# Kernel tuning notes

Hardware: AMD Instinct MI355X
Metric: run time of the kernel (lower is better)

## Reference

```python
import jax, jax.numpy as jnp
import numpy as np

# Faithful JAX port of the approxmatch algorithm (Fan et al. / PyTorch-EMDLoss CUDA kernel):
# iterative soft bipartite matching with annealed temperature levels -4^j for j=8..-1, then 0,
# tracking remaining capacities ('saturation') of both point sets.

EPS = 1e-9

def _approx_match(xyz1, xyz2):
    # xyz1: [B,N,D], xyz2: [B,M,D] -> match: [B,N,M]
    B, n, _ = xyz1.shape
    m = xyz2.shape[1]
    factorl = max(n, m) // n  # capacity per point in set 1
    factorr = max(n, m) // m  # capacity per point in set 2
    # pairwise squared distances [B,N,M]
    d2 = jnp.sum((xyz1[:, :, None, :] - xyz2[:, None, :, :]) ** 2, axis=-1)
    # annealing levels: -4^8, -4^7, ..., -4^-1, 0
    levels = jnp.array([-(4.0 ** j) for j in range(8, -2, -1)] + [0.0],
                       dtype=xyz1.dtype)
    satl0 = jnp.full((B, n), float(factorl), dtype=xyz1.dtype)
    satr0 = jnp.full((B, m), float(factorr), dtype=xyz1.dtype)
    match0 = jnp.zeros((B, n, m), dtype=xyz1.dtype)

    def step(carry, level):
        satl, satr, match = carry
        # soft assignment weights scaled by remaining capacity of set 2
        w = jnp.exp(level * d2) * satr[:, None, :]                      # [B,N,M]
        # row-normalize, scaled by remaining capacity of set 1
        w = w / (jnp.sum(w, axis=2, keepdims=True) + EPS) * satl[:, :, None]
        # column capacity clipping
        ss = jnp.sum(w, axis=1) + EPS                                   # [B,M]
        r = jnp.minimum(satr / ss, 1.0)
        w = w * r[:, None, :]
        satr = jnp.maximum(satr - jnp.sum(w, axis=1), 0.0)
        satl = jnp.maximum(satl - jnp.sum(w, axis=2), 0.0)
        return (satl, satr, match + w), None

    (_, _, match), _ = jax.lax.scan(step, (satl0, satr0, match0), levels)
    return match


def setup_inputs() -> dict:
    key = jax.random.key(0)
    k1, k2 = jax.random.split(key)
    xyz1 = jax.random.normal(k1, (8, 2048, 3), dtype=jnp.float32)
    xyz2 = jax.random.normal(k2, (8, 2048, 3), dtype=jnp.float32)
    return {"xyz1": xyz1, "xyz2": xyz2}


def reference(xyz1, xyz2):
    # EMD cost per batch element: sum_{k,l} match[k,l] * ||x1_k - x2_l||
    match = _approx_match(xyz1, xyz2)                                   # [B,N,M]
    d = jnp.sqrt(jnp.sum((xyz1[:, :, None, :] - xyz2[:, None, :, :]) ** 2,
                         axis=-1))                                      # [B,N,M]
    return jnp.sum(match * d, axis=(1, 2))                              # [B]
```

## Files before the change

kernel.cpp:

```cpp
#include <hip/hip_runtime.h>
#include <math.h>

static constexpr int   B_   = 8;
static constexpr int   N_   = 2048;
static constexpr int   TPB  = 256;
static constexpr int   TILE = 32;
static constexpr int   NBLK = (B_ * N_) / TILE;
static constexpr int   BN   = B_ * N_;
static constexpr float EPS_ = 1e-9f;
static constexpr float LOG2E = 1.4426950408889634f;

#define WS_X1    (ws)
#define WS_X2    (ws + 4*BN)
#define WS_SATL  (ws + 8*BN)
#define WS_SATR  (ws + 9*BN)
#define WS_SCAL  (ws + 10*BN)
#define WS_LSCAL (ws + 11*BN)
#define WS_WLS   (reinterpret_cast<float2*>(ws + 12*BN))
#define WS_WR    (ws + 14*BN)
#define WS_COST  (ws + 15*BN)
#define WS_COSTP (ws + 16*BN)

__global__ void __launch_bounds__(TPB)
emd_init(const float* __restrict__ xyz1, const float* __restrict__ xyz2,
         float* __restrict__ ws)
{
    const int idx = blockIdx.x * TPB + threadIdx.x;
    if (idx >= BN) return;
    float x = xyz1[idx*3], y = xyz1[idx*3+1], z = xyz1[idx*3+2];
    reinterpret_cast<float4*>(WS_X1)[idx] =
        make_float4(x, y, z, fmaf(x,x, fmaf(y,y, z*z)));
    x = xyz2[idx*3]; y = xyz2[idx*3+1]; z = xyz2[idx*3+2];
    reinterpret_cast<float4*>(WS_X2)[idx] =
        make_float4(x, y, z, fmaf(x,x, fmaf(y,y, z*z)));
    WS_SATL[idx] = 1.f;
    WS_SATR[idx] = 1.f;
    WS_COST[idx] = 0.f;
    WS_WLS[idx]  = make_float2(0.f, 0.f);
}

template<int MODE>
__global__ void __launch_bounds__(TPB, (MODE == 2) ? 3 : 4)
emd_pass(float* __restrict__ ws, const float lvlA, const float lvlB)
{
    constexpr int SMEM_BYTES = (MODE == 2) ? (32768 + 16384) : 32768;
    __shared__ __align__(16) char smem[SMEM_BYTES];
    float4* pts  = reinterpret_cast<float4*>(smem);
    float2* aux2 = reinterpret_cast<float2*>(smem + 32768);
    float (*red)[33]  = reinterpret_cast<float(*)[33]>(smem);
    float (*red2)[33] = reinterpret_cast<float(*)[33]>(smem + 64*33*4);

    const int b    = blockIdx.x >> 6;
    const int tile = blockIdx.x & 63;
    const int t    = threadIdx.x;
    const int g    = t & 3;
    const int c    = t >> 2;

    const float4* x1v = reinterpret_cast<const float4*>(WS_X1) + b * N_;
    const float4* x2v = reinterpret_cast<const float4*>(WS_X2) + b * N_;
    const float2* wls = WS_WLS + b * N_;
    const float*  lscal = WS_LSCAL + b * N_;
    const float*  wrp   = WS_WR + b * N_;

    for (int p = t; p < N_; p += TPB) {
        if (MODE == 0) {
            float4 v = x2v[p];
            pts[p] = make_float4(v.x, v.y, v.z, fmaf(lvlB, v.w, wls[p].y));
        } else if (MODE == 1) {
            float4 v = x1v[p];
            pts[p] = make_float4(v.x, v.y, v.z, fmaf(lvlB, v.w, lscal[p]));
        } else if (MODE == 2) {
            float4 v = x2v[p];
            pts[p] = v;
            float2 q = wls[p];
            aux2[p] = make_float2(fmaf(lvlA, v.w, q.x), fmaf(lvlB, v.w, q.y));
        } else {
            float4 v = x2v[p];
            pts[p] = make_float4(v.x, v.y, v.z, wrp[p]);
        }
    }

    const float4* ownv = (MODE == 1) ? x2v : x1v;
    const int ob = tile * TILE + g * 8;
    float kx[8], ky[8], kz[8], kq[8];
#pragma unroll
    for (int j = 0; j < 8; ++j) {
        float4 v = ownv[ob + j];
        if (MODE == 0 || MODE == 1) {
            const float m2lv = -2.f * lvlB;
            kx[j] = m2lv * v.x; ky[j] = m2lv * v.y; kz[j] = m2lv * v.z;
            kq[j] = lvlB * v.w;
        } else if (MODE == 2) {
            kx[j] = -2.f * v.x; ky[j] = -2.f * v.y; kz[j] = -2.f * v.z;
            kq[j] = v.w;
        } else {
            kx[j] = v.x; ky[j] = v.y; kz[j] = v.z; kq[j] = 0.f;
        }
    }
    __syncthreads();

    float s1[8], s2[8], s3[8];
#pragma unroll
    for (int j = 0; j < 8; ++j) { s1[j] = 0.f; s2[j] = 0.f; s3[j] = 0.f; }

    int l = c;
    float4 p = pts[l];
    float2 a;
    if (MODE == 2) a = aux2[l];

    if (MODE == 0 || MODE == 1) {
#pragma unroll 4
        for (int i = 0; i < 32; ++i) {
            const int ln = (l + 64) & (N_ - 1);
            const float4 pn = pts[ln];
#pragma unroll
            for (int j = 0; j < 8; ++j) {
                const float arg = fmaf(kx[j], p.x, fmaf(ky[j], p.y,
                                  fmaf(kz[j], p.z, p.w + kq[j])));
                s1[j] += __builtin_amdgcn_exp2f(arg);
            }
            p = pn; l = ln;
        }
    } else if (MODE == 2) {
#pragma unroll 2
        for (int i = 0; i < 32; ++i) {
            const int ln = (l + 64) & (N_ - 1);
            const float4 pn = pts[ln];
            const float2 an = aux2[ln];
#pragma unroll
            for (int j = 0; j < 8; ++j) {
                const float dq = fmaf(kx[j], p.x, fmaf(ky[j], p.y,
                                 fmaf(kz[j], p.z, kq[j])));
                const float d2 = p.w + dq;
                const float sq = __builtin_amdgcn_sqrtf(fmaxf(d2, 0.f));
                const float eA = __builtin_amdgcn_exp2f(fmaf(lvlA, dq, a.x));
                const float eB = __builtin_amdgcn_exp2f(fmaf(lvlB, dq, a.y));
                s1[j] += eA;
                s2[j]  = fmaf(eA, sq, s2[j]);
                s3[j] += eB;
            }
            p = pn; a = an; l = ln;
        }
    } else {
#pragma unroll 4
        for (int i = 0; i < 32; ++i) {
            const int ln = (l + 64) & (N_ - 1);
            const float4 pn = pts[ln];
#pragma unroll
            for (int j = 0; j < 8; ++j) {
                const float dx = p.x - kx[j], dy = p.y - ky[j], dz = p.z - kz[j];
                const float d2 = fmaf(dx, dx, fmaf(dy, dy, dz * dz));
                const float sq = __builtin_amdgcn_sqrtf(fmaxf(d2, 0.f));
                s2[j] = fmaf(p.w, sq, s2[j]);
            }
            p = pn; l = ln;
        }
    }

#define REDUCE(arr, dst)                                                   \
    {   __syncthreads();                                                   \
        _Pragma("unroll")                                                  \
        for (int j = 0; j < 8; ++j) red[c][g * 8 + j] = arr[j];            \
        __syncthreads();                                                   \
        { const int o = t & 31, sg = t >> 5; float a2 = 0.f;               \
          _Pragma("unroll")                                                \
          for (int k = 0; k < 8; ++k) a2 += red[sg * 8 + k][o];            \
          red2[sg][o] = a2; }                                              \
        __syncthreads();                                                   \
        dst = 0.f;                                                         \
        if (t < TILE) { _Pragma("unroll")                                  \
            for (int sgg = 0; sgg < 8; ++sgg) dst += red2[sgg][t]; } }

    const int gidx = b * N_ + tile * TILE + t;

    if (MODE == 0) {
        float rs1; REDUCE(s1, rs1);
        if (t < TILE) {
            const float sc = WS_SATL[gidx] / (rs1 + EPS_);
            WS_SCAL[gidx]  = sc;
            WS_LSCAL[gidx] = __log2f(sc);
        }
    } else if (MODE == 1) {
        float rs1; REDUCE(s1, rs1);
        if (t < TILE) {
            const float sr  = WS_SATR[gidx];
            const float w1s = sr * rs1;
            const float rr  = fminf(sr / (w1s + EPS_), 1.f);
            const float wrv = sr * rr;
            const float srn = fmaxf(sr - rr * w1s, 0.f);
            WS_SATR[gidx] = srn;
            WS_WR[gidx]   = wrv;
            WS_WLS[gidx + b * N_ * 0] = make_float2(__log2f(wrv), __log2f(srn));
        }
    } else if (MODE == 2) {
        float rs1, rs2, rs3;
        REDUCE(s1, rs1); REDUCE(s2, rs2); REDUCE(s3, rs3);
        if (t < TILE) {
            const float scp = WS_SCAL[gidx];
            const float sln = fmaxf(WS_SATL[gidx] - scp * rs1, 0.f);
            WS_COST[gidx]   = fmaf(scp, rs2, WS_COST[gidx]);
            const float scn = sln / (rs3 + EPS_);
            WS_SATL[gidx]  = sln;
            WS_SCAL[gidx]  = scn;
            WS_LSCAL[gidx] = __log2f(scn);
        }
    } else {
        float rs2; REDUCE(s2, rs2);
        float v = 0.f;
        if (t < TILE)
            v = fmaf(WS_SCAL[gidx], rs2, WS_COST[gidx]);
        if (t < 64) {
#pragma unroll
            for (int k = 16; k >= 1; k >>= 1) v += __shfl_xor(v, k, 64);
            if (t == 0) WS_COSTP[blockIdx.x] = v;
        }
    }
#undef REDUCE
}

__global__ void __launch_bounds__(64)
emd_finish(const float* __restrict__ costp, float* __restrict__ out)
{
    const int b = blockIdx.x;
    const int t = threadIdx.x;
    float v = costp[b * 64 + t];
#pragma unroll
    for (int k = 32; k >= 1; k >>= 1) v += __shfl_xor(v, k, 64);
    if (t == 0) out[b] = v;
}

extern "C" void kernel_launch(void* const* d_in, const int* in_sizes, int n_in,
                              void* d_out, int out_size, void* d_ws, size_t ws_size,
                              hipStream_t stream)
{
    const float* xyz1 = (const float*)d_in[0];
    const float* xyz2 = (const float*)d_in[1];
    float* out = (float*)d_out;
    float* ws  = (float*)d_ws;

    emd_init<<<BN / TPB, TPB, 0, stream>>>(xyz1, xyz2, ws);

    static const float levels[11] = {
        -65536.f, -16384.f, -4096.f, -1024.f, -256.f,
        -64.f, -16.f, -4.f, -1.f, -0.25f, 0.f};

    emd_pass<0><<<NBLK, TPB, 0, stream>>>(ws, 0.f, levels[0] * LOG2E);
    emd_pass<1><<<NBLK, TPB, 0, stream>>>(ws, 0.f, levels[0] * LOG2E);
    for (int lev = 1; lev < 11; ++lev) {
        emd_pass<2><<<NBLK, TPB, 0, stream>>>(ws, levels[lev-1] * LOG2E,
                                                  levels[lev]   * LOG2E);
        emd_pass<1><<<NBLK, TPB, 0, stream>>>(ws, 0.f, levels[lev] * LOG2E);
    }
    emd_pass<3><<<NBLK, TPB, 0, stream>>>(ws, 0.f, 0.f);

    emd_finish<<<B_, 64, 0, stream>>>(WS_COSTP, out);
}
```

Measured before the change: 339.2 us.

## Halve row tile to 16, use packed float2 math, fuse final reduction via atomics

Halves the rows handled per block (16 instead of 32) so each block is split across more threads, doubling the grid to 1024 blocks, and caps occupancy at 4 for every mode. The inner distance math is rewritten with 2-wide vector types so the compiler can emit packed FMA instructions. The MODE 2 LDS footprint is reduced by folding one log term into the point w component. The finish kernel is replaced with atomicAdd into a zero-filled output. The intent is to use the GPU more fully and cut ALU issue per element; the cost is reloading the column points for twice as many blocks, plus nondeterministic float summation order from the atomics.

```diff
diff --git a/kernel.cpp b/kernel.cpp
--- a/kernel.cpp
+++ b/kernel.cpp
@@ -1,11 +1,14 @@
 #include <hip/hip_runtime.h>
 #include <math.h>
+
+typedef float f2 __attribute__((ext_vector_type(2)));
 
 static constexpr int   B_   = 8;
 static constexpr int   N_   = 2048;
 static constexpr int   TPB  = 256;
-static constexpr int   TILE = 32;
-static constexpr int   NBLK = (B_ * N_) / TILE;
+static constexpr int   TILE = 16;
+static constexpr int   BPB  = 128;
+static constexpr int   NBLK = B_ * BPB;
 static constexpr int   BN   = B_ * N_;
 static constexpr float EPS_ = 1e-9f;
 static constexpr float LOG2E = 1.4426950408889634f;
@@ -16,10 +19,10 @@
 #define WS_SATR  (ws + 9*BN)
 #define WS_SCAL  (ws + 10*BN)
 #define WS_LSCAL (ws + 11*BN)
-#define WS_WLS   (reinterpret_cast<float2*>(ws + 12*BN))
+#define WS_LSATR (ws + 12*BN)
+#define WS_LWR   (ws + 13*BN)
 #define WS_WR    (ws + 14*BN)
 #define WS_COST  (ws + 15*BN)
-#define WS_COSTP (ws + 16*BN)
 
 __global__ void __launch_bounds__(TPB)
 emd_init(const float* __restrict__ xyz1, const float* __restrict__ xyz2,
@@ -33,47 +36,81 @@
     x = xyz2[idx*3]; y = xyz2[idx*3+1]; z = xyz2[idx*3+2];
     reinterpret_cast<float4*>(WS_X2)[idx] =
         make_float4(x, y, z, fmaf(x,x, fmaf(y,y, z*z)));
-    WS_SATL[idx] = 1.f;
-    WS_SATR[idx] = 1.f;
-    WS_COST[idx] = 0.f;
-    WS_WLS[idx]  = make_float2(0.f, 0.f);
+    WS_SATL[idx]  = 1.f;
+    WS_SATR[idx]  = 1.f;
+    WS_LSATR[idx] = 0.f;
+    WS_COST[idx]  = 0.f;
+}
+
+template<int NA>
+__device__ __forceinline__ void reduce_multi(float* sc, const float (*s)[8],
+                                             int t, float* rs)
+{
+    const int c = t >> 1, g = t & 1;
+    __syncthreads();
+#pragma unroll
+    for (int a = 0; a < NA; ++a) {
+        float* red = sc + a * 2176;
+#pragma unroll
+        for (int j = 0; j < 8; ++j) red[c*17 + g*8 + j] = s[a][j];
+    }
+    __syncthreads();
+    {
+        const int col = t & 15, seg = t >> 4;
+#pragma unroll
+        for (int a = 0; a < NA; ++a) {
+            const float* red = sc + a * 2176;
+            float v = 0.f;
+#pragma unroll
+            for (int k = 0; k < 8; ++k) v += red[(seg*8 + k)*17 + col];
+            sc[6528 + a*272 + seg*17 + col] = v;
+        }
+    }
+    __syncthreads();
+    if (t < 16) {
+#pragma unroll
+        for (int a = 0; a < NA; ++a) {
+            float r = 0.f;
+#pragma unroll
+            for (int q = 0; q < 16; ++q) r += sc[6528 + a*272 + q*17 + t];
+            rs[a] = r;
+        }
+    }
 }
 
 template<int MODE>
-__global__ void __launch_bounds__(TPB, (MODE == 2) ? 3 : 4)
-emd_pass(float* __restrict__ ws, const float lvlA, const float lvlB)
-{
-    constexpr int SMEM_BYTES = (MODE == 2) ? (32768 + 16384) : 32768;
-    __shared__ __align__(16) char smem[SMEM_BYTES];
+__global__ void __launch_bounds__(TPB, 4)
+emd_pass(float* __restrict__ ws, float* __restrict__ out,
+         const float lvA, const float lvB)
+{
+    constexpr int SMEM = (MODE == 2) ? 40960 : 32768;
+    __shared__ __align__(16) char smem[SMEM];
     float4* pts  = reinterpret_cast<float4*>(smem);
-    float2* aux2 = reinterpret_cast<float2*>(smem + 32768);
-    float (*red)[33]  = reinterpret_cast<float(*)[33]>(smem);
-    float (*red2)[33] = reinterpret_cast<float(*)[33]>(smem + 64*33*4);
-
-    const int b    = blockIdx.x >> 6;
-    const int tile = blockIdx.x & 63;
+    float*  auxB = reinterpret_cast<float*>(smem + 32768);
+    float*  sc   = reinterpret_cast<float*>(smem);
+
+    const int b    = blockIdx.x >> 7;
+    const int tile = blockIdx.x & 127;
     const int t    = threadIdx.x;
-    const int g    = t & 3;
-    const int c    = t >> 2;
 
     const float4* x1v = reinterpret_cast<const float4*>(WS_X1) + b * N_;
     const float4* x2v = reinterpret_cast<const float4*>(WS_X2) + b * N_;
-    const float2* wls = WS_WLS + b * N_;
-    const float*  lscal = WS_LSCAL + b * N_;
-    const float*  wrp   = WS_WR + b * N_;
+    const float* lscal = WS_LSCAL + b * N_;
+    const float* lsatr = WS_LSATR + b * N_;
+    const float* lwr   = WS_LWR   + b * N_;
+    const float* wrp   = WS_WR    + b * N_;
 
     for (int p = t; p < N_; p += TPB) {
         if (MODE == 0) {
             float4 v = x2v[p];
-            pts[p] = make_float4(v.x, v.y, v.z, fmaf(lvlB, v.w, wls[p].y));
+            pts[p] = make_float4(v.x, v.y, v.z, lvB * v.w);
         } else if (MODE == 1) {
             float4 v = x1v[p];
-            pts[p] = make_float4(v.x, v.y, v.z, fmaf(lvlB, v.w, lscal[p]));
+            pts[p] = make_float4(v.x, v.y, v.z, fmaf(lvB, v.w, lscal[p]));
         } else if (MODE == 2) {
             float4 v = x2v[p];
-            pts[p] = v;
-            float2 q = wls[p];
-            aux2[p] = make_float2(fmaf(lvlA, v.w, q.x), fmaf(lvlB, v.w, q.y));
+            pts[p]  = make_float4(v.x, v.y, v.z, fmaf(lvA, v.w, lwr[p]));
+            auxB[p] = fmaf(lvB, v.w, lsatr[p]);
         } else {
             float4 v = x2v[p];
             pts[p] = make_float4(v.x, v.y, v.z, wrp[p]);
@@ -81,20 +118,22 @@
     }
 
     const float4* ownv = (MODE == 1) ? x2v : x1v;
-    const int ob = tile * TILE + g * 8;
-    float kx[8], ky[8], kz[8], kq[8];
-#pragma unroll
-    for (int j = 0; j < 8; ++j) {
-        float4 v = ownv[ob + j];
+    const int ob = tile * TILE + (t & 1) * 8;
+    f2 kx[4], ky[4], kz[4], kc[4];
+#pragma unroll
+    for (int jp = 0; jp < 4; ++jp) {
+        float4 v0 = ownv[ob + 2*jp], v1 = ownv[ob + 2*jp + 1];
         if (MODE == 0 || MODE == 1) {
-            const float m2lv = -2.f * lvlB;
-            kx[j] = m2lv * v.x; ky[j] = m2lv * v.y; kz[j] = m2lv * v.z;
-            kq[j] = lvlB * v.w;
-        } else if (MODE == 2) {
-            kx[j] = -2.f * v.x; ky[j] = -2.f * v.y; kz[j] = -2.f * v.z;
-            kq[j] = v.w;
+            const float m2 = -2.f * lvB;
+            kx[jp] = (f2){m2*v0.x, m2*v1.x};
+            ky[jp] = (f2){m2*v0.y, m2*v1.y};
+            kz[jp] = (f2){m2*v0.z, m2*v1.z};
+            kc[jp] = (f2){lvB*v0.w, lvB*v1.w};
         } else {
-            kx[j] = v.x; ky[j] = v.y; kz[j] = v.z; kq[j] = 0.f;
+            kx[jp] = (f2){-2.f*v0.x, -2.f*v1.x};
+            ky[jp] = (f2){-2.f*v0.y, -2.f*v1.y};
+            kz[jp] = (f2){-2.f*v0.z, -2.f*v1.z};
+            kc[jp] = (f2){v0.w, v1.w};
         }
     }
     __syncthreads();
@@ -103,130 +142,110 @@
 #pragma unroll
     for (int j = 0; j < 8; ++j) { s1[j] = 0.f; s2[j] = 0.f; s3[j] = 0.f; }
 
-    int l = c;
+    int l = t >> 1;
     float4 p = pts[l];
-    float2 a;
-    if (MODE == 2) a = aux2[l];
-
-    if (MODE == 0 || MODE == 1) {
-#pragma unroll 4
-        for (int i = 0; i < 32; ++i) {
-            const int ln = (l + 64) & (N_ - 1);
-            const float4 pn = pts[ln];
-#pragma unroll
-            for (int j = 0; j < 8; ++j) {
-                const float arg = fmaf(kx[j], p.x, fmaf(ky[j], p.y,
-                                  fmaf(kz[j], p.z, p.w + kq[j])));
-                s1[j] += __builtin_amdgcn_exp2f(arg);
+    float  ab = (MODE == 2) ? auxB[l] : 0.f;
+
+#pragma unroll 2
+    for (int i = 0; i < 16; ++i) {
+        const int ln = (l + 128) & (N_ - 1);
+        const float4 pn = pts[ln];
+        float abn = 0.f;
+        if (MODE == 2) abn = auxB[ln];
+
+        const f2 px = (f2){p.x, p.x}, py = (f2){p.y, p.y}, pz = (f2){p.z, p.z};
+        float p2s = 0.f;
+        if (MODE == 2 || MODE == 3)
+            p2s = fmaf(p.x, p.x, fmaf(p.y, p.y, p.z * p.z));
+
+#pragma unroll
+        for (int jp = 0; jp < 4; ++jp) {
+            if (MODE == 0 || MODE == 1) {
+                f2 a = kc[jp] + (f2){p.w, p.w};
+                a = kz[jp] * pz + a;
+                a = ky[jp] * py + a;
+                a = kx[jp] * px + a;
+                s1[2*jp]   += __builtin_amdgcn_exp2f(a.x);
+                s1[2*jp+1] += __builtin_amdgcn_exp2f(a.y);
+            } else if (MODE == 2) {
+                f2 dq = kz[jp] * pz + kc[jp];
+                dq = ky[jp] * py + dq;
+                dq = kx[jp] * px + dq;
+                const float d20 = dq.x + p2s, d21 = dq.y + p2s;
+                const float sq0 = __builtin_amdgcn_sqrtf(fmaxf(d20, 0.f));
+                const float sq1 = __builtin_amdgcn_sqrtf(fmaxf(d21, 0.f));
+                const float eA0 = __builtin_amdgcn_exp2f(fmaf(lvA, dq.x, p.w));
+                const float eA1 = __builtin_amdgcn_exp2f(fmaf(lvA, dq.y, p.w));
+                const float eB0 = __builtin_amdgcn_exp2f(fmaf(lvB, dq.x, ab));
+                const float eB1 = __builtin_amdgcn_exp2f(fmaf(lvB, dq.y, ab));
+                s1[2*jp]   += eA0;            s1[2*jp+1] += eA1;
+                s2[2*jp]    = fmaf(eA0, sq0, s2[2*jp]);
+                s2[2*jp+1]  = fmaf(eA1, sq1, s2[2*jp+1]);
+                s3[2*jp]   += eB0;            s3[2*jp+1] += eB1;
+            } else {
+                f2 dq = kz[jp] * pz + kc[jp];
+                dq = ky[jp] * py + dq;
+                dq = kx[jp] * px + dq;
+                const float sq0 = __builtin_amdgcn_sqrtf(fmaxf(dq.x + p2s, 0.f));
+                const float sq1 = __builtin_amdgcn_sqrtf(fmaxf(dq.y + p2s, 0.f));
+                s2[2*jp]   = fmaf(p.w, sq0, s2[2*jp]);
+                s2[2*jp+1] = fmaf(p.w, sq1, s2[2*jp+1]);
             }
-            p = pn; l = ln;
-        }
-    } else if (MODE == 2) {
-#pragma unroll 2
-        for (int i = 0; i < 32; ++i) {
-            const int ln = (l + 64) & (N_ - 1);
-            const float4 pn = pts[ln];
-            const float2 an = aux2[ln];
-#pragma unroll
-            for (int j = 0; j < 8; ++j) {
-                const float dq = fmaf(kx[j], p.x, fmaf(ky[j], p.y,
-                                 fmaf(kz[j], p.z, kq[j])));
-                const float d2 = p.w + dq;
-                const float sq = __builtin_amdgcn_sqrtf(fmaxf(d2, 0.f));
-                const float eA = __builtin_amdgcn_exp2f(fmaf(lvlA, dq, a.x));
-                const float eB = __builtin_amdgcn_exp2f(fmaf(lvlB, dq, a.y));
-                s1[j] += eA;
-                s2[j]  = fmaf(eA, sq, s2[j]);
-                s3[j] += eB;
-            }
-            p = pn; a = an; l = ln;
-        }
-    } else {
-#pragma unroll 4
-        for (int i = 0; i < 32; ++i) {
-            const int ln = (l + 64) & (N_ - 1);
-            const float4 pn = pts[ln];
-#pragma unroll
-            for (int j = 0; j < 8; ++j) {
-                const float dx = p.x - kx[j], dy = p.y - ky[j], dz = p.z - kz[j];
-                const float d2 = fmaf(dx, dx, fmaf(dy, dy, dz * dz));
-                const float sq = __builtin_amdgcn_sqrtf(fmaxf(d2, 0.f));
-                s2[j] = fmaf(p.w, sq, s2[j]);
-            }
-            p = pn; l = ln;
-        }
-    }
-
-#define REDUCE(arr, dst)                                                   \
-    {   __syncthreads();                                                   \
-        _Pragma("unroll")                                                  \
-        for (int j = 0; j < 8; ++j) red[c][g * 8 + j] = arr[j];            \
-        __syncthreads();                                                   \
-        { const int o = t & 31, sg = t >> 5; float a2 = 0.f;               \
-          _Pragma("unroll")                                                \
-          for (int k = 0; k < 8; ++k) a2 += red[sg * 8 + k][o];            \
-          red2[sg][o] = a2; }                                              \
-        __syncthreads();                                                   \
-        dst = 0.f;                                                         \
-        if (t < TILE) { _Pragma("unroll")                                  \
-            for (int sgg = 0; sgg < 8; ++sgg) dst += red2[sgg][t]; } }
+        }
+        p = pn; ab = abn; l = ln;
+    }
 
     const int gidx = b * N_ + tile * TILE + t;
 
     if (MODE == 0) {
-        float rs1; REDUCE(s1, rs1);
+        float rs[1];
+        reduce_multi<1>(sc, &s1, t, rs);
         if (t < TILE) {
-            const float sc = WS_SATL[gidx] / (rs1 + EPS_);
-            WS_SCAL[gidx]  = sc;
-            WS_LSCAL[gidx] = __log2f(sc);
+            const float scv = WS_SATL[gidx] / (rs[0] + EPS_);
+            WS_SCAL[gidx]  = scv;
+            WS_LSCAL[gidx] = __log2f(scv);
         }
     } else if (MODE == 1) {
-        float rs1; REDUCE(s1, rs1);
+        float rs[1];
+        reduce_multi<1>(sc, &s1, t, rs);
         if (t < TILE) {
             const float sr  = WS_SATR[gidx];
-            const float w1s = sr * rs1;
+            const float w1s = sr * rs[0];
             const float rr  = fminf(sr / (w1s + EPS_), 1.f);
             const float wrv = sr * rr;
             const float srn = fmaxf(sr - rr * w1s, 0.f);
-            WS_SATR[gidx] = srn;
-            WS_WR[gidx]   = wrv;
-            WS_WLS[gidx + b * N_ * 0] = make_float2(__log2f(wrv), __log2f(srn));
+            WS_SATR[gidx]  = srn;
+            WS_WR[gidx]    = wrv;
+            WS_LWR[gidx]   = __log2f(wrv);
+            WS_LSATR[gidx] = __log2f(srn);
         }
     } else if (MODE == 2) {
-        float rs1, rs2, rs3;
-        REDUCE(s1, rs1); REDUCE(s2, rs2); REDUCE(s3, rs3);
+        float sall[3][8];
+#pragma unroll
+        for (int j = 0; j < 8; ++j) {
+            sall[0][j] = s1[j]; sall[1][j] = s2[j]; sall[2][j] = s3[j];
+        }
+        float rs[3];
+        reduce_multi<3>(sc, sall, t, rs);
         if (t < TILE) {
             const float scp = WS_SCAL[gidx];
-            const float sln = fmaxf(WS_SATL[gidx] - scp * rs1, 0.f);
-            WS_COST[gidx]   = fmaf(scp, rs2, WS_COST[gidx]);
-            const float scn = sln / (rs3 + EPS_);
+            const float sln = fmaxf(WS_SATL[gidx] - scp * rs[0], 0.f);
+            WS_COST[gidx]   = fmaf(scp, rs[1], WS_COST[gidx]);
+            const float scn = sln / (rs[2] + EPS_);
             WS_SATL[gidx]  = sln;
             WS_SCAL[gidx]  = scn;
             WS_LSCAL[gidx] = __log2f(scn);
         }
     } else {
-        float rs2; REDUCE(s2, rs2);
-        float v = 0.f;
-        if (t < TILE)
-            v = fmaf(WS_SCAL[gidx], rs2, WS_COST[gidx]);
-        if (t < 64) {
-#pragma unroll
-            for (int k = 16; k >= 1; k >>= 1) v += __shfl_xor(v, k, 64);
-            if (t == 0) WS_COSTP[blockIdx.x] = v;
-        }
-    }
-#undef REDUCE
-}
-
-__global__ void __launch_bounds__(64)
-emd_finish(const float* __restrict__ costp, float* __restrict__ out)
-{
-    const int b = blockIdx.x;
-    const int t = threadIdx.x;
-    float v = costp[b * 64 + t];
-#pragma unroll
-    for (int k = 32; k >= 1; k >>= 1) v += __shfl_xor(v, k, 64);
-    if (t == 0) out[b] = v;
+        float rs[1];
+        reduce_multi<1>(sc, &s2, t, rs);
+        if (t < 16) {
+            float v = fmaf(WS_SCAL[gidx], rs[0], WS_COST[gidx]);
+#pragma unroll
+            for (int k = 8; k >= 1; k >>= 1) v += __shfl_xor(v, k, 16);
+            if (t == 0) atomicAdd(out + b, v);
+        }
+    }
 }
 
 extern "C" void kernel_launch(void* const* d_in, const int* in_sizes, int n_in,
@@ -238,20 +257,19 @@
     float* out = (float*)d_out;
     float* ws  = (float*)d_ws;
 
+    hipMemsetAsync(d_out, 0, B_ * sizeof(float), stream);
     emd_init<<<BN / TPB, TPB, 0, stream>>>(xyz1, xyz2, ws);
 
     static const float levels[11] = {
         -65536.f, -16384.f, -4096.f, -1024.f, -256.f,
         -64.f, -16.f, -4.f, -1.f, -0.25f, 0.f};
 
-    emd_pass<0><<<NBLK, TPB, 0, stream>>>(ws, 0.f, levels[0] * LOG2E);
-    emd_pass<1><<<NBLK, TPB, 0, stream>>>(ws, 0.f, levels[0] * LOG2E);
+    emd_pass<0><<<NBLK, TPB, 0, stream>>>(ws, out, 0.f, levels[0] * LOG2E);
+    emd_pass<1><<<NBLK, TPB, 0, stream>>>(ws, out, 0.f, levels[0] * LOG2E);
     for (int lev = 1; lev < 11; ++lev) {
-        emd_pass<2><<<NBLK, TPB, 0, stream>>>(ws, levels[lev-1] * LOG2E,
-                                                  levels[lev]   * LOG2E);
-        emd_pass<1><<<NBLK, TPB, 0, stream>>>(ws, 0.f, levels[lev] * LOG2E);
-    }
-    emd_pass<3><<<NBLK, TPB, 0, stream>>>(ws, 0.f, 0.f);
-
-    emd_finish<<<B_, 64, 0, stream>>>(WS_COSTP, out);
-}
+        emd_pass<2><<<NBLK, TPB, 0, stream>>>(ws, out, levels[lev-1] * LOG2E,
+                                                       levels[lev]   * LOG2E);
+        emd_pass<1><<<NBLK, TPB, 0, stream>>>(ws, out, 0.f, levels[lev] * LOG2E);
+    }
+    emd_pass<3><<<NBLK, TPB, 0, stream>>>(ws, out, 0.f, 0.f);
+}
```

Result: faster. 320.5 us, median of 2 (-5.5%).
